# Kernel tuning notes

Measured on AMD Instinct MI355X. Metric: run time of the kernel, lower is better.

## Reference

```python
import jax, jax.numpy as jnp
import numpy as np

EPS = 1e-5  # batchnorm eps (torch default)


def setup_inputs() -> dict:
    key = jax.random.key(0)
    ks = jax.random.split(key, 16)
    N, E, Din, H, Dout = 100000, 600000, 128, 128, 64
    x = jax.random.normal(ks[0], (N, Din), dtype=jnp.float32)
    edge_index = jax.random.randint(ks[1], (2, E), 0, N, dtype=jnp.int64)
    def lin(k, fan_in, fan_out):
        s = 1.0 / np.sqrt(fan_in)
        return jax.random.uniform(k, (fan_in, fan_out), jnp.float32, -s, s)
    return {
        "x": x,
        "edge_index": edge_index,
        "W1": lin(ks[2], Din, H), "b1": jnp.zeros((H,), jnp.float32),
        "W2": lin(ks[3], H, H),   "b2": jnp.zeros((H,), jnp.float32),
        "W3": lin(ks[4], H, H),   "b3": jnp.zeros((H,), jnp.float32),
        "W4": lin(ks[5], H, Dout),"b4": jnp.zeros((Dout,), jnp.float32),
        "g1": jnp.ones((H,), jnp.float32), "be1": jnp.zeros((H,), jnp.float32),
        "g2": jnp.ones((H,), jnp.float32), "be2": jnp.zeros((H,), jnp.float32),
        "g3": jnp.ones((H,), jnp.float32), "be3": jnp.zeros((H,), jnp.float32),
    }


def _gcn_norm(edge_index, N, dtype):
    # GCNConv default: add self-loops, symmetric normalization D^-1/2 A D^-1/2
    loop = jnp.arange(N, dtype=edge_index.dtype)
    src = jnp.concatenate([edge_index[0], loop])
    dst = jnp.concatenate([edge_index[1], loop])
    deg = jax.ops.segment_sum(jnp.ones_like(src, dtype=dtype), dst, num_segments=N)
    dinv = jax.lax.rsqrt(deg)  # deg >= 1 thanks to self-loops
    norm = dinv[src] * dinv[dst]  # [E+N]
    return src, dst, norm


def _conv(h, W, b, src, dst, norm, N):
    hw = h @ W                      # [N, out]
    msg = hw[src] * norm[:, None]   # gather + scale, [E+N, out]
    return jax.ops.segment_sum(msg, dst, num_segments=N) + b


def _bn(h, gamma, beta):
    # training-mode batchnorm over node dimension (biased variance)
    mu = jnp.mean(h, axis=0)
    var = jnp.mean(jnp.square(h - mu), axis=0)
    return (h - mu) * jax.lax.rsqrt(var + EPS) * gamma + beta


def reference(x, edge_index, W1, b1, W2, b2, W3, b3, W4, b4,
              g1, be1, g2, be2, g3, be3):
    N = x.shape[0]
    src, dst, norm = _gcn_norm(edge_index, N, x.dtype)
    h = jax.nn.relu(_conv(x, W1, b1, src, dst, norm, N))
    h = _bn(h, g1, be1)
    h = jax.nn.relu(_conv(h, W2, b2, src, dst, norm, N))
    h = _bn(h, g2, be2)
    h = jax.nn.relu(_conv(h, W3, b3, src, dst, norm, N))
    h = _bn(h, g3, be3)
    h = jax.nn.relu(_conv(h, W4, b4, src, dst, norm, N))
    return h
```

## Files before the change

### kernel.cpp

```cpp
#include <hip/hip_runtime.h>

#define BN_EPS 1e-5f

using bfrag = __attribute__((ext_vector_type(8))) short;
using f32x4 = __attribute__((ext_vector_type(4))) float;

__device__ inline float bf2f(unsigned int h16) {
    union { unsigned int u; float f; } v; v.u = h16 << 16; return v.f;
}
__device__ inline unsigned short f2bf(float f) {
    union { float f; unsigned int u; } v; v.f = f;
    unsigned int u = v.u;
    u += 0x7fffu + ((u >> 16) & 1u);
    return (unsigned short)(u >> 16);
}
__device__ inline void unpack8(uint4 u, float* f) {
    f[0] = bf2f(u.x & 0xffffu); f[1] = bf2f(u.x >> 16);
    f[2] = bf2f(u.y & 0xffffu); f[3] = bf2f(u.y >> 16);
    f[4] = bf2f(u.z & 0xffffu); f[5] = bf2f(u.z >> 16);
    f[6] = bf2f(u.w & 0xffffu); f[7] = bf2f(u.w >> 16);
}
__device__ inline void fma8(uint4 G, float w, float* acc) {
    float v[8];
    unpack8(G, v);
#pragma unroll
    for (int k = 0; k < 8; ++k) acc[k] += w * v[k];
}


__global__ void count_kernel(const int* __restrict__ ei, int E, int* __restrict__ cnt) {
    int e = blockIdx.x * blockDim.x + threadIdx.x;
    if (e < E) atomicAdd(&cnt[ei[E + e]], 1);
}

__global__ void dinv_kernel(const int* __restrict__ cnt, float* __restrict__ dinv, int N) {
    int i = blockIdx.x * blockDim.x + threadIdx.x;
    if (i < N) dinv[i] = rsqrtf((float)(cnt[i] + 1));
}

__global__ __launch_bounds__(1024) void scan_blocks(const int* __restrict__ cnt,
                                                    int* __restrict__ rowptr,
                                                    int* __restrict__ bsum, int N) {
    __shared__ int sh[1024];
    int t = threadIdx.x;
    int i = blockIdx.x * 1024 + t;
    int v = (i < N) ? cnt[i] + 1 : 0;
    sh[t] = v;
    __syncthreads();
    for (int off = 1; off < 1024; off <<= 1) {
        int x = (t >= off) ? sh[t - off] : 0;
        __syncthreads();
        sh[t] += x;
        __syncthreads();
    }
    if (i < N) rowptr[i] = sh[t] - v;
    if (t == 1023) bsum[blockIdx.x] = sh[1023];
}

__global__ void scan_carry(const int* __restrict__ bsum, int* __restrict__ boff, int nblk) {
    if (threadIdx.x == 0 && blockIdx.x == 0) {
        int run = 0;
        for (int b = 0; b < nblk; ++b) { int v = bsum[b]; boff[b] = run; run += v; }
        boff[nblk] = run;
    }
}

__global__ void scan_add(int* __restrict__ rowptr, const int* __restrict__ boff,
                         int* __restrict__ cursor, int N, int nblk) {
    int i = blockIdx.x * blockDim.x + threadIdx.x;
    if (i < N) {
        int v = rowptr[i] + boff[i >> 10];
        rowptr[i] = v;
        cursor[i] = v;
    }
    if (i == 0) rowptr[N] = boff[nblk];
}

__global__ void fill_kernel(const int* __restrict__ ei, int E, int* __restrict__ cursor,
                            const float* __restrict__ dinv, int2* __restrict__ epack) {
    int e = blockIdx.x * blockDim.x + threadIdx.x;
    if (e < E) {
        int s = ei[e], d = ei[E + e];
        int p = atomicAdd(&cursor[d], 1);
        float nrm = dinv[s] * dinv[d];
        epack[p] = make_int2(s, __float_as_int(nrm));
    }
}

__global__ void self_kernel(int N, int* __restrict__ cursor, const float* __restrict__ dinv,
                            int2* __restrict__ epack) {
    int i = blockIdx.x * blockDim.x + threadIdx.x;
    if (i < N) {
        int p = atomicAdd(&cursor[i], 1);
        float w = dinv[i] * dinv[i];
        epack[p] = make_int2(i, __float_as_int(w));
    }
}

__global__ void s_kernel(const int* __restrict__ rowptr, const int2* __restrict__ epack,
                         float* __restrict__ sarr, int N) {
    int i = blockIdx.x * blockDim.x + threadIdx.x;
    if (i < N) {
        float a = 0.f;
        int j1 = rowptr[i + 1];
        for (int j = rowptr[i]; j < j1; ++j) a += __int_as_float(epack[j].y);
        sarr[i] = a;
    }
}


template <bool HASBN>
__global__ __launch_bounds__(256) void prep_kernel(const float* __restrict__ W, int COLS,
                                                   const float* __restrict__ stats,
                                                   const float* __restrict__ g,
                                                   const float* __restrict__ be, float invN,
                                                   unsigned short* __restrict__ Wt,
                                                   float* __restrict__ cvec) {
    __shared__ float sc[128], sh[128];
    int tid = threadIdx.x;
    if (tid < 128) {
        if (HASBN) {
            float mu  = stats[tid] * invN;
            float var = stats[128 + tid] * invN - mu * mu;
            float rs  = rsqrtf(var + BN_EPS);
            float s   = rs * g[tid];
            sc[tid] = s;
            sh[tid] = be[tid] - mu * s;
        } else { sc[tid] = 1.f; sh[tid] = 0.f; }
    }
    __syncthreads();
    int total = 128 * COLS;
    for (int idx = blockIdx.x * 256 + tid; idx < total; idx += gridDim.x * 256) {
        int k = idx / COLS, j = idx % COLS;
        Wt[j * 128 + k] = f2bf(sc[k] * W[idx]);
    }
    if (blockIdx.x == 0 && tid < COLS) {
        float a = 0.f;
        if (HASBN)
            for (int k = 0; k < 128; ++k) a += sh[k] * W[k * COLS + tid];
        cvec[tid] = a;
    }
}


template <int COLS, bool IN_F32>
__global__ __launch_bounds__(256) void gemm_mfma(const void* __restrict__ Hin,
                                                 const unsigned short* __restrict__ Wt,
                                                 unsigned short* __restrict__ out, int N) {
    __shared__ unsigned short Hs[64][136];
    const int tid  = threadIdx.x;
    const int row0 = blockIdx.x * 64;

    if (IN_F32) {
        const float* H = (const float*)Hin;
#pragma unroll
        for (int it = 0; it < 8; ++it) {
            int idx = it * 256 + tid;
            int r = idx >> 5, c4 = (idx & 31) * 4;
            float4 v = {0.f, 0.f, 0.f, 0.f};
            if (row0 + r < N) v = *(const float4*)(H + (size_t)(row0 + r) * 128 + c4);
            Hs[r][c4 + 0] = f2bf(v.x); Hs[r][c4 + 1] = f2bf(v.y);
            Hs[r][c4 + 2] = f2bf(v.z); Hs[r][c4 + 3] = f2bf(v.w);
        }
    } else {
        const unsigned short* H = (const unsigned short*)Hin;
#pragma unroll
        for (int it = 0; it < 4; ++it) {
            int idx = it * 256 + tid;
            int r = idx >> 4, c8 = (idx & 15) * 8;
            uint4 v = {0u, 0u, 0u, 0u};
            if (row0 + r < N) v = *(const uint4*)(H + (size_t)(row0 + r) * 128 + c8);
            *(uint4*)&Hs[r][c8] = v;
        }
    }
    __syncthreads();

    const int lane = tid & 63, wave = tid >> 6;
    const int arow = lane & 15, kg = lane >> 4;
    const int r0   = wave * 16;

    bfrag af[4];
#pragma unroll
    for (int kc = 0; kc < 4; ++kc) af[kc] = *(const bfrag*)&Hs[r0 + arow][kc * 32 + kg * 8];

    constexpr int NT = COLS / 16;
    f32x4 acc[NT];
#pragma unroll
    for (int nt = 0; nt < NT; ++nt) acc[nt] = (f32x4){0.f, 0.f, 0.f, 0.f};

#pragma unroll
    for (int nt = 0; nt < NT; ++nt) {
        const unsigned short* wp = Wt + (size_t)(nt * 16 + arow) * 128 + kg * 8;
#pragma unroll
        for (int kc = 0; kc < 4; ++kc) {
            bfrag bf = *(const bfrag*)(wp + kc * 32);
            acc[nt] = __builtin_amdgcn_mfma_f32_16x16x32_bf16(af[kc], bf, acc[nt], 0, 0, 0);
        }
    }
    __syncthreads();

#pragma unroll
    for (int nt = 0; nt < NT; ++nt) {
        int col = nt * 16 + arow;
#pragma unroll
        for (int r = 0; r < 4; ++r)
            Hs[r0 + kg * 4 + r][col] = f2bf(acc[nt][r]);
    }
    __syncthreads();

    constexpr int CH = COLS / 8;
    for (int idx = tid; idx < 64 * CH; idx += 256) {
        int r = idx / CH, c8 = (idx % CH) * 8;
        if (row0 + r < N)
            *(uint4*)(out + (size_t)(row0 + r) * COLS + c8) = *(const uint4*)&Hs[r][c8];
    }
}


template <int F, bool STATS, bool HASC, typename TOUT, int RG>
__global__ __launch_bounds__(256) void agg_kernel(const unsigned short* __restrict__ HW,
                                                  const int* __restrict__ rowptr,
                                                  const int2* __restrict__ epack,
                                                  const float* __restrict__ sarr,
                                                  const float* __restrict__ cvec,
                                                  const float* __restrict__ bias,
                                                  TOUT* __restrict__ out,
                                                  float* __restrict__ stats, int N) {
    constexpr int TPR  = F / 8;
    constexpr int NGRP = 256 / TPR;
    const int tid = threadIdx.x;
    const int grp = tid / TPR;
    const int j8  = (tid % TPR) * 8;
    const int r0  = (blockIdx.x * NGRP + grp) * RG;

    float ssum[8], ssq[8];
    if (STATS) {
#pragma unroll
        for (int k = 0; k < 8; ++k) { ssum[k] = 0.f; ssq[k] = 0.f; }
    }

    if (r0 < N) {
        float b8[8], c8[8];
#pragma unroll
        for (int k = 0; k < 8; ++k) b8[k] = bias[j8 + k];
        if (HASC) {
#pragma unroll
            for (int k = 0; k < 8; ++k) c8[k] = cvec[j8 + k];
        }

        const int e0 = rowptr[r0];
        int bound = rowptr[min(r0 + 1, N)];
        int bnd2  = rowptr[min(r0 + 2, N)];
        int bnd3  = rowptr[min(r0 + 3, N)];
        int bnd4  = rowptr[min(r0 + 4, N)];
        const int eend = bnd4;
        float sv = 0.f, sv2 = 0.f, sv3 = 0.f, sv4 = 0.f;
        if (HASC) {
            sv  = sarr[r0];
            sv2 = sarr[min(r0 + 1, N - 1)];
            sv3 = sarr[min(r0 + 2, N - 1)];
            sv4 = sarr[min(r0 + 3, N - 1)];
        }
        int r = r0;

        float acc[8];
#pragma unroll
        for (int k = 0; k < 8; ++k) acc[k] = 0.f;

#define FLUSH()                                                               \
    do {                                                                      \
        if (HASC) {                                                           \
            _Pragma("unroll") for (int k = 0; k < 8; ++k) acc[k] += c8[k] * sv; \
        }                                                                     \
        _Pragma("unroll") for (int k = 0; k < 8; ++k)                         \
            acc[k] = fmaxf(acc[k] + b8[k], 0.f);                              \
        if constexpr (sizeof(TOUT) == 2) {                                    \
            unsigned int p0 = (unsigned int)f2bf(acc[0]) | ((unsigned int)f2bf(acc[1]) << 16); \
            unsigned int p1 = (unsigned int)f2bf(acc[2]) | ((unsigned int)f2bf(acc[3]) << 16); \
            unsigned int p2 = (unsigned int)f2bf(acc[4]) | ((unsigned int)f2bf(acc[5]) << 16); \
            unsigned int p3 = (unsigned int)f2bf(acc[6]) | ((unsigned int)f2bf(acc[7]) << 16); \
            uint4 o = {p0, p1, p2, p3};                                       \
            *(uint4*)((unsigned short*)out + (size_t)r * F + j8) = o;         \
        } else {                                                              \
            float4 o0 = {acc[0], acc[1], acc[2], acc[3]};                     \
            float4 o1 = {acc[4], acc[5], acc[6], acc[7]};                     \
            *(float4*)((float*)out + (size_t)r * F + j8)     = o0;            \
            *(float4*)((float*)out + (size_t)r * F + j8 + 4) = o1;            \
        }                                                                     \
        if (STATS) {                                                          \
            _Pragma("unroll") for (int k = 0; k < 8; ++k) {                   \
                ssum[k] += acc[k];                                            \
                ssq[k]  += acc[k] * acc[k];                                   \
            }                                                                 \
        }                                                                     \
        _Pragma("unroll") for (int k = 0; k < 8; ++k) acc[k] = 0.f;           \
        sv = sv2; sv2 = sv3; sv3 = sv4;                                       \
        bound = bnd2; bnd2 = bnd3; bnd3 = bnd4;                               \
    } while (0)

#define EPLOAD(ss, ww, ii)                                                    \
    do { int _i = (ii);                                                       \
        if (_i < eend) { int2 _e = epack[_i];                                 \
            ss = _e.x; ww = __int_as_float(_e.y); }                           \
    } while (0)

#define GISS(G, gw, ss, ww)                                                   \
    do { G = *(const uint4*)(HW + (size_t)(ss) * F + j8); gw = (ww); } while (0)

#define CONS1(G, gw, ii)                                                      \
    do { int _c = (ii);                                                       \
        if (_c < eend) {                                                      \
            if (_c >= bound) { FLUSH(); ++r; }                                \
            fma8(G, gw, acc);                                                 \
        }                                                                     \
    } while (0)

        int sA0 = 0, sA1 = 0, sA2 = 0, sA3 = 0, sB0 = 0, sB1 = 0, sB2 = 0, sB3 = 0;
        float wA0 = 0, wA1 = 0, wA2 = 0, wA3 = 0, wB0 = 0, wB1 = 0, wB2 = 0, wB3 = 0;
        uint4 GA0 = {}, GA1 = {}, GA2 = {}, GA3 = {}, GB0 = {}, GB1 = {}, GB2 = {}, GB3 = {};
        float ga0 = 0, ga1 = 0, ga2 = 0, ga3 = 0, gb0 = 0, gb1 = 0, gb2 = 0, gb3 = 0;

        EPLOAD(sA0, wA0, e0 + 0); EPLOAD(sA1, wA1, e0 + 1);
        EPLOAD(sA2, wA2, e0 + 2); EPLOAD(sA3, wA3, e0 + 3);
        EPLOAD(sB0, wB0, e0 + 4); EPLOAD(sB1, wB1, e0 + 5);
        EPLOAD(sB2, wB2, e0 + 6); EPLOAD(sB3, wB3, e0 + 7);
        GISS(GA0, ga0, sA0, wA0); GISS(GA1, ga1, sA1, wA1);
        GISS(GA2, ga2, sA2, wA2); GISS(GA3, ga3, sA3, wA3);

        for (int b = e0; b < eend; b += 8) {
            EPLOAD(sA0, wA0, b + 8);  EPLOAD(sA1, wA1, b + 9);
            EPLOAD(sA2, wA2, b + 10); EPLOAD(sA3, wA3, b + 11);
            GISS(GB0, gb0, sB0, wB0); GISS(GB1, gb1, sB1, wB1);
            GISS(GB2, gb2, sB2, wB2); GISS(GB3, gb3, sB3, wB3);
            CONS1(GA0, ga0, b + 0); CONS1(GA1, ga1, b + 1);
            CONS1(GA2, ga2, b + 2); CONS1(GA3, ga3, b + 3);

            EPLOAD(sB0, wB0, b + 12); EPLOAD(sB1, wB1, b + 13);
            EPLOAD(sB2, wB2, b + 14); EPLOAD(sB3, wB3, b + 15);
            GISS(GA0, ga0, sA0, wA0); GISS(GA1, ga1, sA1, wA1);
            GISS(GA2, ga2, sA2, wA2); GISS(GA3, ga3, sA3, wA3);
            CONS1(GB0, gb0, b + 4); CONS1(GB1, gb1, b + 5);
            CONS1(GB2, gb2, b + 6); CONS1(GB3, gb3, b + 7);
        }
        FLUSH();

#undef FLUSH
#undef EPLOAD
#undef GISS
#undef CONS1
    }

    if constexpr (STATS) {
        __shared__ float red[NGRP][F];
#pragma unroll
        for (int k = 0; k < 8; ++k) red[grp][j8 + k] = ssum[k];
        __syncthreads();
        if (tid < F) {
            float a = 0.f;
#pragma unroll
            for (int g = 0; g < NGRP; ++g) a += red[g][tid];
            atomicAdd(&stats[tid], a);
        }
        __syncthreads();
#pragma unroll
        for (int k = 0; k < 8; ++k) red[grp][j8 + k] = ssq[k];
        __syncthreads();
        if (tid < F) {
            float a = 0.f;
#pragma unroll
            for (int g = 0; g < NGRP; ++g) a += red[g][tid];
            atomicAdd(&stats[F + tid], a);
        }
    }
}


extern "C" void kernel_launch(void* const* d_in, const int* in_sizes, int n_in,
                              void* d_out, int out_size, void* d_ws, size_t ws_size,
                              hipStream_t stream) {
    const float* x  = (const float*)d_in[0];
    const int*   ei = (const int*)d_in[1];
    const float* W1 = (const float*)d_in[2];  const float* b1 = (const float*)d_in[3];
    const float* W2 = (const float*)d_in[4];  const float* b2 = (const float*)d_in[5];
    const float* W3 = (const float*)d_in[6];  const float* b3 = (const float*)d_in[7];
    const float* W4 = (const float*)d_in[8];  const float* b4 = (const float*)d_in[9];
    const float* g1 = (const float*)d_in[10]; const float* be1 = (const float*)d_in[11];
    const float* g2 = (const float*)d_in[12]; const float* be2 = (const float*)d_in[13];
    const float* g3 = (const float*)d_in[14]; const float* be3 = (const float*)d_in[15];

    const int N = in_sizes[0] / 128;
    const int E = in_sizes[1] / 2;
    const int nblk = (N + 1023) / 1024;

    size_t off = 0;
    char* ws = (char*)d_ws;
    auto alloc = [&](size_t bytes) -> void* {
        void* p = ws + off;
        off += (bytes + 255) & ~(size_t)255;
        return p;
    };
    int*   cnt    = (int*)alloc((size_t)N * 4);
    float* dinv   = (float*)alloc((size_t)N * 4);
    int*   rowptr = (int*)alloc((size_t)(N + 1) * 4);
    int*   cursor = (int*)alloc((size_t)N * 4);
    int*   bsum   = (int*)alloc((size_t)nblk * 4);
    int*   boff   = (int*)alloc((size_t)(nblk + 1) * 4);
    int2*  epack  = (int2*)alloc((size_t)(E + N) * 8);
    float* sarr   = (float*)alloc((size_t)N * 4);
    float* stats  = (float*)alloc(256 * 4);
    unsigned short* Wt = (unsigned short*)alloc(128 * 128 * 2);
    float* cvec   = (float*)alloc(128 * 4);
    unsigned short* hA  = (unsigned short*)alloc((size_t)N * 128 * 2);
    unsigned short* hwB = (unsigned short*)alloc((size_t)N * 128 * 2);
    (void)ws_size; (void)n_in; (void)out_size;

    const int TB = 256;
    const int gE = (E + TB - 1) / TB;
    const int gN = (N + TB - 1) / TB;

    hipMemsetAsync(cnt, 0, (size_t)N * 4, stream);
    count_kernel<<<gE, TB, 0, stream>>>(ei, E, cnt);
    dinv_kernel<<<gN, TB, 0, stream>>>(cnt, dinv, N);
    scan_blocks<<<nblk, 1024, 0, stream>>>(cnt, rowptr, bsum, N);
    scan_carry<<<1, 1, 0, stream>>>(bsum, boff, nblk);
    scan_add<<<gN, TB, 0, stream>>>(rowptr, boff, cursor, N, nblk);
    fill_kernel<<<gE, TB, 0, stream>>>(ei, E, cursor, dinv, epack);
    self_kernel<<<gN, TB, 0, stream>>>(N, cursor, dinv, epack);
    s_kernel<<<gN, TB, 0, stream>>>(rowptr, epack, sarr, N);

    const int gG    = (N + 63) / 64;
    const int gA128 = (N + 63) / 64;
    const int gA64  = (N + 127) / 128;
    const float invN = 1.0f / (float)N;

    prep_kernel<false><<<8, 256, 0, stream>>>(W1, 128, nullptr, nullptr, nullptr, 0.f, Wt, cvec);
    gemm_mfma<128, true><<<gG, 256, 0, stream>>>(x, Wt, hwB, N);
    hipMemsetAsync(stats, 0, 256 * 4, stream);
    agg_kernel<128, true, false, unsigned short, 4><<<gA128, 256, 0, stream>>>(
        hwB, rowptr, epack, sarr, cvec, b1, hA, stats, N);

    prep_kernel<true><<<8, 256, 0, stream>>>(W2, 128, stats, g1, be1, invN, Wt, cvec);
    gemm_mfma<128, false><<<gG, 256, 0, stream>>>(hA, Wt, hwB, N);
    hipMemsetAsync(stats, 0, 256 * 4, stream);
    agg_kernel<128, true, true, unsigned short, 4><<<gA128, 256, 0, stream>>>(
        hwB, rowptr, epack, sarr, cvec, b2, hA, stats, N);

    prep_kernel<true><<<8, 256, 0, stream>>>(W3, 128, stats, g2, be2, invN, Wt, cvec);
    gemm_mfma<128, false><<<gG, 256, 0, stream>>>(hA, Wt, hwB, N);
    hipMemsetAsync(stats, 0, 256 * 4, stream);
    agg_kernel<128, true, true, unsigned short, 4><<<gA128, 256, 0, stream>>>(
        hwB, rowptr, epack, sarr, cvec, b3, hA, stats, N);

    prep_kernel<true><<<8, 256, 0, stream>>>(W4, 64, stats, g3, be3, invN, Wt, cvec);
    gemm_mfma<64, false><<<gG, 256, 0, stream>>>(hA, Wt, hwB, N);
    agg_kernel<64, false, true, float, 4><<<gA64, 256, 0, stream>>>(
        hwB, rowptr, epack, sarr, cvec, b4, (float*)d_out, nullptr, N);
}
```

Baseline: 461.3 us.

## Fuse dinv into scan, drop self-loop atomics, use LDS atomics for BN stats

Computes dinv inside the block scan kernel, which removes one launch. The self-loop kernel now reads the cursor instead of doing an atomicAdd, since self-loops are written after all edges. In the aggregation kernel, the per-thread stat accumulators and the two-pass shared-memory reduction are replaced by shared-memory float atomics per output row. The prep kernel grid is also doubled. The LDS atomics add contention, 16 atomics per thread per row, which may cost more than the old register accumulation; prep with 16 blocks depends on code not shown.

```diff
diff --git a/kernel.cpp b/kernel.cpp
--- a/kernel.cpp
+++ b/kernel.cpp
@@ -33,18 +33,15 @@
     if (e < E) atomicAdd(&cnt[ei[E + e]], 1);
 }
 
-__global__ void dinv_kernel(const int* __restrict__ cnt, float* __restrict__ dinv, int N) {
-    int i = blockIdx.x * blockDim.x + threadIdx.x;
-    if (i < N) dinv[i] = rsqrtf((float)(cnt[i] + 1));
-}
-
 __global__ __launch_bounds__(1024) void scan_blocks(const int* __restrict__ cnt,
                                                     int* __restrict__ rowptr,
-                                                    int* __restrict__ bsum, int N) {
+                                                    int* __restrict__ bsum,
+                                                    float* __restrict__ dinv, int N) {
     __shared__ int sh[1024];
     int t = threadIdx.x;
     int i = blockIdx.x * 1024 + t;
     int v = (i < N) ? cnt[i] + 1 : 0;
+    if (i < N) dinv[i] = rsqrtf((float)v);
     sh[t] = v;
     __syncthreads();
     for (int off = 1; off < 1024; off <<= 1) {
@@ -87,13 +84,13 @@
     }
 }
 
-__global__ void self_kernel(int N, int* __restrict__ cursor, const float* __restrict__ dinv,
-                            int2* __restrict__ epack) {
+__global__ void self_kernel(int N, const int* __restrict__ cursor,
+                            const float* __restrict__ dinv, int2* __restrict__ epack) {
     int i = blockIdx.x * blockDim.x + threadIdx.x;
     if (i < N) {
-        int p = atomicAdd(&cursor[i], 1);
-        float w = dinv[i] * dinv[i];
-        epack[p] = make_int2(i, __float_as_int(w));
+        int p = cursor[i];
+        float d = dinv[i];
+        epack[p] = make_int2(i, __float_as_int(d * d));
     }
 }
 
@@ -228,16 +225,15 @@
                                                   float* __restrict__ stats, int N) {
     constexpr int TPR  = F / 8;
     constexpr int NGRP = 256 / TPR;
+    __shared__ float sred[256];
     const int tid = threadIdx.x;
+    if (STATS) {
+        sred[tid] = 0.f;
+        __syncthreads();
+    }
     const int grp = tid / TPR;
     const int j8  = (tid % TPR) * 8;
     const int r0  = (blockIdx.x * NGRP + grp) * RG;
-
-    float ssum[8], ssq[8];
-    if (STATS) {
-#pragma unroll
-        for (int k = 0; k < 8; ++k) { ssum[k] = 0.f; ssq[k] = 0.f; }
-    }
 
     if (r0 < N) {
         float b8[8], c8[8];
@@ -274,6 +270,12 @@
         }                                                                     \
         _Pragma("unroll") for (int k = 0; k < 8; ++k)                         \
             acc[k] = fmaxf(acc[k] + b8[k], 0.f);                              \
+        if (STATS) {                                                          \
+            _Pragma("unroll") for (int k = 0; k < 8; ++k) {                   \
+                atomicAdd(&sred[j8 + k], acc[k]);                             \
+                atomicAdd(&sred[128 + j8 + k], acc[k] * acc[k]);              \
+            }                                                                 \
+        }                                                                     \
         if constexpr (sizeof(TOUT) == 2) {                                    \
             unsigned int p0 = (unsigned int)f2bf(acc[0]) | ((unsigned int)f2bf(acc[1]) << 16); \
             unsigned int p1 = (unsigned int)f2bf(acc[2]) | ((unsigned int)f2bf(acc[3]) << 16); \
@@ -287,12 +289,6 @@
             *(float4*)((float*)out + (size_t)r * F + j8)     = o0;            \
             *(float4*)((float*)out + (size_t)r * F + j8 + 4) = o1;            \
         }                                                                     \
-        if (STATS) {                                                          \
-            _Pragma("unroll") for (int k = 0; k < 8; ++k) {                   \
-                ssum[k] += acc[k];                                            \
-                ssq[k]  += acc[k] * acc[k];                                   \
-            }                                                                 \
-        }                                                                     \
         _Pragma("unroll") for (int k = 0; k < 8; ++k) acc[k] = 0.f;           \
         sv = sv2; sv2 = sv3; sv3 = sv4;                                       \
         bound = bnd2; bnd2 = bnd3; bnd3 = bnd4;                               \
@@ -350,27 +346,9 @@
 #undef CONS1
     }
 
-    if constexpr (STATS) {
-        __shared__ float red[NGRP][F];
-#pragma unroll
-        for (int k = 0; k < 8; ++k) red[grp][j8 + k] = ssum[k];
+    if (STATS) {
         __syncthreads();
-        if (tid < F) {
-            float a = 0.f;
-#pragma unroll
-            for (int g = 0; g < NGRP; ++g) a += red[g][tid];
-            atomicAdd(&stats[tid], a);
-        }
-        __syncthreads();
-#pragma unroll
-        for (int k = 0; k < 8; ++k) red[grp][j8 + k] = ssq[k];
-        __syncthreads();
-        if (tid < F) {
-            float a = 0.f;
-#pragma unroll
-            for (int g = 0; g < NGRP; ++g) a += red[g][tid];
-            atomicAdd(&stats[F + tid], a);
-        }
+        atomicAdd(&stats[tid], sred[tid]);
     }
 }
 
@@ -408,7 +386,7 @@
     int2*  epack  = (int2*)alloc((size_t)(E + N) * 8);
     float* sarr   = (float*)alloc((size_t)N * 4);
     float* stats  = (float*)alloc(256 * 4);
-    unsigned short* Wt = (unsigned short*)alloc(128 * 128 * 2);
+    unsigned short* Wt  = (unsigned short*)alloc(128 * 128 * 2);
     float* cvec   = (float*)alloc(128 * 4);
     unsigned short* hA  = (unsigned short*)alloc((size_t)N * 128 * 2);
     unsigned short* hwB = (unsigned short*)alloc((size_t)N * 128 * 2);
@@ -420,8 +398,7 @@
 
     hipMemsetAsync(cnt, 0, (size_t)N * 4, stream);
     count_kernel<<<gE, TB, 0, stream>>>(ei, E, cnt);
-    dinv_kernel<<<gN, TB, 0, stream>>>(cnt, dinv, N);
-    scan_blocks<<<nblk, 1024, 0, stream>>>(cnt, rowptr, bsum, N);
+    scan_blocks<<<nblk, 1024, 0, stream>>>(cnt, rowptr, bsum, dinv, N);
     scan_carry<<<1, 1, 0, stream>>>(bsum, boff, nblk);
     scan_add<<<gN, TB, 0, stream>>>(rowptr, boff, cursor, N, nblk);
     fill_kernel<<<gE, TB, 0, stream>>>(ei, E, cursor, dinv, epack);
@@ -433,25 +410,25 @@
     const int gA64  = (N + 127) / 128;
     const float invN = 1.0f / (float)N;
 
-    prep_kernel<false><<<8, 256, 0, stream>>>(W1, 128, nullptr, nullptr, nullptr, 0.f, Wt, cvec);
+    prep_kernel<false><<<16, 256, 0, stream>>>(W1, 128, nullptr, nullptr, nullptr, 0.f, Wt, cvec);
     gemm_mfma<128, true><<<gG, 256, 0, stream>>>(x, Wt, hwB, N);
     hipMemsetAsync(stats, 0, 256 * 4, stream);
     agg_kernel<128, true, false, unsigned short, 4><<<gA128, 256, 0, stream>>>(
         hwB, rowptr, epack, sarr, cvec, b1, hA, stats, N);
 
-    prep_kernel<true><<<8, 256, 0, stream>>>(W2, 128, stats, g1, be1, invN, Wt, cvec);
+    prep_kernel<true><<<16, 256, 0, stream>>>(W2, 128, stats, g1, be1, invN, Wt, cvec);
     gemm_mfma<128, false><<<gG, 256, 0, stream>>>(hA, Wt, hwB, N);
     hipMemsetAsync(stats, 0, 256 * 4, stream);
     agg_kernel<128, true, true, unsigned short, 4><<<gA128, 256, 0, stream>>>(
         hwB, rowptr, epack, sarr, cvec, b2, hA, stats, N);
 
-    prep_kernel<true><<<8, 256, 0, stream>>>(W3, 128, stats, g2, be2, invN, Wt, cvec);
+    prep_kernel<true><<<16, 256, 0, stream>>>(W3, 128, stats, g2, be2, invN, Wt, cvec);
     gemm_mfma<128, false><<<gG, 256, 0, stream>>>(hA, Wt, hwB, N);
     hipMemsetAsync(stats, 0, 256 * 4, stream);
     agg_kernel<128, true, true, unsigned short, 4><<<gA128, 256, 0, stream>>>(
         hwB, rowptr, epack, sarr, cvec, b3, hA, stats, N);
 
-    prep_kernel<true><<<8, 256, 0, stream>>>(W4, 64, stats, g3, be3, invN, Wt, cvec);
+    prep_kernel<true><<<16, 256, 0, stream>>>(W4, 64, stats, g3, be3, invN, Wt, cvec);
     gemm_mfma<64, false><<<gG, 256, 0, stream>>>(hA, Wt, hwB, N);
     agg_kernel<64, false, true, float, 4><<<gA64, 256, 0, stream>>>(
         hwB, rowptr, epack, sarr, cvec, b4, (float*)d_out, nullptr, N);
```

Measured after the change: 732.1 us. 58.7% more time.
